# Kernel tuning notes

Measured on AMD Instinct MI355X. Metric: run time of the kernel, lower is better.

Reference implementation:

```python
import jax, jax.numpy as jnp
import numpy as np
from jax.ops import segment_sum

NUM_EMBEDDINGS = 512
EMBEDDING_DIM = 64
COMMITMENT_COST = 0.25
DECAY = 0.99
EPSILON = 1e-05


def setup_inputs() -> dict:
    key = jax.random.key(0)
    k1, k2, k3 = jax.random.split(key, 3)
    B, C, T = 32, EMBEDDING_DIM, 4096
    z = jax.random.normal(k1, (B, C, T), dtype=jnp.float32)
    embedding = jax.random.normal(k2, (NUM_EMBEDDINGS, EMBEDDING_DIM), dtype=jnp.float32)
    cluster_size = jnp.zeros((NUM_EMBEDDINGS,), dtype=jnp.float32)
    embed_avg = jax.random.normal(k3, (NUM_EMBEDDINGS, EMBEDDING_DIM), dtype=jnp.float32)
    return {"z": z, "embedding": embedding, "cluster_size": cluster_size, "embed_avg": embed_avg}


def reference(z, embedding, cluster_size, embed_avg):
    B, C, T = z.shape
    K = embedding.shape[0]
    # flatten: (B, C, T) -> (B*T, C), matching reshape(B,C,-1).permute(0,2,1).reshape(-1,C)
    z_flat = jnp.transpose(z, (0, 2, 1)).reshape(-1, C)  # [N, C]
    N = z_flat.shape[0]

    # squared-euclidean nearest-code search (argmin of cdist == argmin of sq dist)
    d2 = (jnp.sum(z_flat * z_flat, axis=1, keepdims=True)
          - 2.0 * (z_flat @ embedding.T)
          + jnp.sum(embedding * embedding, axis=1)[None, :])  # [N, K]
    indices = jnp.argmin(d2, axis=1)  # [N] int

    # quantize: gather instead of one-hot matmul (same math)
    quantized_flat = embedding[indices]  # [N, C]
    quantized = jnp.transpose(quantized_flat.reshape(B, T, C), (0, 2, 1))  # [B, C, T]

    # EMA codebook update (training branch)
    n = segment_sum(jnp.ones((N,), dtype=z.dtype), indices, num_segments=K)  # [K]
    new_cluster_size = cluster_size * DECAY + (1.0 - DECAY) * n
    embed_sum = segment_sum(z_flat, indices, num_segments=K)  # [K, C]
    new_embed_avg = embed_avg * DECAY + (1.0 - DECAY) * embed_sum
    n_tot = jnp.sum(new_cluster_size)
    cs_smoothed = (new_cluster_size + EPSILON) / (n_tot + K * EPSILON) * n_tot
    new_embedding = new_embed_avg / cs_smoothed[:, None]

    # commitment loss against detached quantized
    commitment_loss = jnp.mean((z - jax.lax.stop_gradient(quantized)) ** 2)
    vq_loss = COMMITMENT_COST * commitment_loss

    # straight-through estimator
    quantized_st = z + jax.lax.stop_gradient(quantized - z)

    # perplexity over code usage (zero-count codes contribute ~0, as in torch unique version)
    probs = n / N
    perplexity = jnp.exp(-jnp.sum(probs * jnp.log(probs + 1e-10)))

    return (quantized_st, indices, vq_loss, perplexity,
            new_embedding, new_cluster_size, new_embed_avg)
```

## Files before the change

### kernel.cpp

```cpp
#include <hip/hip_runtime.h>
#include <math.h>

#define KB_NUM 512
#define DIMC 64
#define BSZ 32
#define TLEN 4096
#define NTOK (BSZ * TLEN)
#define DECAY_F 0.99f
#define EPS_F 1e-5f

#define Q_OFF    ((size_t)0)
#define IDX_OFF  ((size_t)BSZ * DIMC * TLEN)
#define LOSS_OFF (IDX_OFF + (size_t)NTOK)
#define PLEX_OFF (LOSS_OFF + 1)
#define NEMB_OFF (PLEX_OFF + 1)
#define NCS_OFF  (NEMB_OFF + (size_t)KB_NUM * DIMC)
#define NEA_OFF  (NCS_OFF + (size_t)KB_NUM)

typedef _Float16 f16x8 __attribute__((ext_vector_type(8)));
typedef float    f32x4 __attribute__((ext_vector_type(4)));

__global__ __launch_bounds__(64) void vq_prep_e(
    const float* __restrict__ emb,
    _Float16* __restrict__ efrag,
    float* __restrict__ enorm)
{
    const int k = blockIdx.x;
    const int c = threadIdx.x;
    float v = emb[(size_t)k * DIMC + c];
    _Float16 h = (_Float16)v;
    _Float16 l = (_Float16)(v - (float)h);

    const int kgrp = k >> 4, row = k & 15;
    const int ks = c >> 5, seg = (c & 31) >> 3, j = c & 7;
    const int lane = seg * 16 + row;
    const size_t base = ((size_t)(kgrp * 2 + ks) * 2) * 512;
    efrag[base + (size_t)lane * 8 + j]       = h;
    efrag[base + 512 + (size_t)lane * 8 + j] = l;

    float s = v * v;
    #pragma unroll
    for (int off = 32; off > 0; off >>= 1)
        s += __shfl_down(s, off, 64);
    if (c == 0) enorm[k] = 0.5f * s;
}

#define LOADA(P, kg) do {                                                     \
    const _Float16* fb_ = efrag + ((size_t)((kg) & 31) * 4) * 512             \
                                + (size_t)ln * 8;                             \
    P##h0 = *(const f16x8*)(fb_);                                             \
    P##l0 = *(const f16x8*)(fb_ + 512);                                       \
    P##h1 = *(const f16x8*)(fb_ + 1024);                                      \
    P##l1 = *(const f16x8*)(fb_ + 1536);                                      \
} while (0)

#define CONSUME(P, ct) do {                                                   \
    _Pragma("unroll")                                                         \
    for (int tt = 0; tt < 4; ++tt)                                            \
        acc[ct][tt] = __builtin_amdgcn_mfma_f32_16x16x32_f16(                 \
            P##h0, zhf[tt][0], acc[ct][tt], 0, 0, 0);                         \
    _Pragma("unroll")                                                         \
    for (int tt = 0; tt < 4; ++tt)                                            \
        acc[ct][tt] = __builtin_amdgcn_mfma_f32_16x16x32_f16(                 \
            P##h0, zlf[tt][0], acc[ct][tt], 0, 0, 0);                         \
    _Pragma("unroll")                                                         \
    for (int tt = 0; tt < 4; ++tt)                                            \
        acc[ct][tt] = __builtin_amdgcn_mfma_f32_16x16x32_f16(                 \
            P##l0, zhf[tt][0], acc[ct][tt], 0, 0, 0);                         \
    _Pragma("unroll")                                                         \
    for (int tt = 0; tt < 4; ++tt)                                            \
        acc[ct][tt] = __builtin_amdgcn_mfma_f32_16x16x32_f16(                 \
            P##l0, zlf[tt][0], acc[ct][tt], 0, 0, 0);                         \
    _Pragma("unroll")                                                         \
    for (int tt = 0; tt < 4; ++tt)                                            \
        acc[ct][tt] = __builtin_amdgcn_mfma_f32_16x16x32_f16(                 \
            P##h1, zhf[tt][1], acc[ct][tt], 0, 0, 0);                         \
    _Pragma("unroll")                                                         \
    for (int tt = 0; tt < 4; ++tt)                                            \
        acc[ct][tt] = __builtin_amdgcn_mfma_f32_16x16x32_f16(                 \
            P##h1, zlf[tt][1], acc[ct][tt], 0, 0, 0);                         \
    _Pragma("unroll")                                                         \
    for (int tt = 0; tt < 4; ++tt)                                            \
        acc[ct][tt] = __builtin_amdgcn_mfma_f32_16x16x32_f16(                 \
            P##l1, zhf[tt][1], acc[ct][tt], 0, 0, 0);                         \
    _Pragma("unroll")                                                         \
    for (int tt = 0; tt < 4; ++tt)                                            \
        acc[ct][tt] = __builtin_amdgcn_mfma_f32_16x16x32_f16(                 \
            P##l1, zlf[tt][1], acc[ct][tt], 0, 0, 0);                         \
} while (0)

__global__ __launch_bounds__(256, 2) void vq_main_kernel(
    const float* __restrict__ z,
    const float* __restrict__ emb,
    const _Float16* __restrict__ efrag,
    const float* __restrict__ enorm,
    float* __restrict__ out,
    float* __restrict__ lossAcc)
{
    __shared__ float zs[256 * 65];
    __shared__ float sen[KB_NUM];

    const int tid = threadIdx.x;
    const int w   = tid >> 6;
    const int ln  = tid & 63;
    const int bk  = blockIdx.x;
    const int b   = bk >> 4;
    const int t0  = (bk & 15) << 8;

    sen[tid]       = enorm[tid];
    sen[tid + 256] = enorm[tid + 256];

    const float* zg = z + (size_t)b * (DIMC * TLEN) + t0;

    #pragma unroll 8
    for (int c = 0; c < DIMC; ++c)
        zs[tid * 65 + c] = zg[(size_t)c * TLEN + tid];
    __syncthreads();

    f16x8 zhf[4][2], zlf[4][2];
    #pragma unroll
    for (int tt = 0; tt < 4; ++tt) {
        #pragma unroll
        for (int ks = 0; ks < 2; ++ks) {
            const float* zrow = &zs[(w * 64 + tt * 16 + (ln & 15)) * 65
                                    + ks * 32 + ((ln >> 4) << 3)];
            #pragma unroll
            for (int j = 0; j < 8; ++j) {
                float v = zrow[j];
                _Float16 h = (_Float16)v;
                zhf[tt][ks][j] = h;
                zlf[tt][ks][j] = (_Float16)(v - (float)h);
            }
        }
    }

    float bv[4] = {3.4e38f, 3.4e38f, 3.4e38f, 3.4e38f};
    int   bi[4] = {0, 0, 0, 0};

    f16x8 A0h0, A0l0, A0h1, A0l1;
    f16x8 A1h0, A1l0, A1h1, A1l1;
    LOADA(A0, 0);
    LOADA(A1, 1);

    #pragma unroll 1
    for (int chunk = 0; chunk < 8; ++chunk) {
        const int kb = chunk * 4;
        f32x4 acc[4][4];
        #pragma unroll
        for (int ct = 0; ct < 4; ++ct)
            #pragma unroll
            for (int tt = 0; tt < 4; ++tt)
                acc[ct][tt] = (f32x4){0.f, 0.f, 0.f, 0.f};

        CONSUME(A0, 0); LOADA(A0, kb + 2);
        CONSUME(A1, 1); LOADA(A1, kb + 3);
        CONSUME(A0, 2); LOADA(A0, kb + 4);
        CONSUME(A1, 3); LOADA(A1, kb + 5);

        #pragma unroll
        for (int ct = 0; ct < 4; ++ct) {
            const int cb = chunk * 64 + ct * 16 + ((ln >> 4) << 2);
            float4 en = *(const float4*)&sen[cb];
            const float e0 = en.x, e1 = en.y, e2 = en.z, e3 = en.w;
            #pragma unroll
            for (int tt = 0; tt < 4; ++tt) {
                float s0 = e0 - acc[ct][tt][0];
                float s1 = e1 - acc[ct][tt][1];
                float s2 = e2 - acc[ct][tt][2];
                float s3 = e3 - acc[ct][tt][3];
                if (s0 < bv[tt]) { bv[tt] = s0; bi[tt] = cb; }
                if (s1 < bv[tt]) { bv[tt] = s1; bi[tt] = cb + 1; }
                if (s2 < bv[tt]) { bv[tt] = s2; bi[tt] = cb + 2; }
                if (s3 < bv[tt]) { bv[tt] = s3; bi[tt] = cb + 3; }
            }
        }
    }

    #pragma unroll
    for (int mask = 16; mask <= 32; mask <<= 1) {
        #pragma unroll
        for (int tt = 0; tt < 4; ++tt) {
            float ov = __shfl_xor(bv[tt], mask, 64);
            int   oi = __shfl_xor(bi[tt], mask, 64);
            if (ov < bv[tt] || (ov == bv[tt] && oi < bi[tt])) {
                bv[tt] = ov; bi[tt] = oi;
            }
        }
    }

    const int g = ln >> 4;
    const int idxv = (g == 0) ? bi[0] : (g == 1) ? bi[1] : (g == 2) ? bi[2] : bi[3];
    const int tok = w * 64 + ln;

    out[IDX_OFF + (size_t)b * TLEN + t0 + tok] = (float)idxv;

    const float* er   = emb + (size_t)idxv * DIMC;
    const float* zrow = &zs[tok * 65];
    float* qo = out + (size_t)b * (DIMC * TLEN) + t0 + tok;

    float lsum = 0.f;
    #pragma unroll
    for (int c4 = 0; c4 < DIMC / 4; ++c4) {
        float4 ev = *(const float4*)(er + c4 * 4);
        float z0 = zrow[c4 * 4 + 0], z1 = zrow[c4 * 4 + 1];
        float z2 = zrow[c4 * 4 + 2], z3 = zrow[c4 * 4 + 3];
        float d0 = ev.x - z0, d1 = ev.y - z1, d2 = ev.z - z2, d3 = ev.w - z3;
        qo[(size_t)(c4 * 4 + 0) * TLEN] = z0 + d0;
        qo[(size_t)(c4 * 4 + 1) * TLEN] = z1 + d1;
        qo[(size_t)(c4 * 4 + 2) * TLEN] = z2 + d2;
        qo[(size_t)(c4 * 4 + 3) * TLEN] = z3 + d3;
        lsum = fmaf(d0, d0, lsum); lsum = fmaf(d1, d1, lsum);
        lsum = fmaf(d2, d2, lsum); lsum = fmaf(d3, d3, lsum);
    }

    #pragma unroll
    for (int off = 32; off > 0; off >>= 1)
        lsum += __shfl_down(lsum, off, 64);
    if (ln == 0) atomicAdd(lossAcc, lsum);
}

__global__ __launch_bounds__(512, 1) void vq_bin_kernel(
    const float* __restrict__ z,
    const float* __restrict__ out,
    float* __restrict__ cnt,
    float* __restrict__ esum,
    int R)
{
    __shared__ float acc[KB_NUM][DIMC + 1];
    __shared__ float zs[64][DIMC + 1];
    __shared__ float scnt[KB_NUM];
    __shared__ int   idxbuf[64];

    const int tid = threadIdx.x;
    const int w   = tid >> 6;
    const int ln  = tid & 63;

    for (int j = tid; j < KB_NUM * (DIMC + 1); j += 512) ((float*)acc)[j] = 0.f;
    if (tid < KB_NUM) scnt[tid] = 0.f;
    __syncthreads();

    const int b   = blockIdx.x >> 3;
    const int tb  = (blockIdx.x & 7) * 512;
    const float* zp = z + (size_t)b * (DIMC * TLEN) + tb;
    const size_t gib = IDX_OFF + (size_t)b * TLEN + tb;

    #pragma unroll 1
    for (int ch = 0; ch < 8; ++ch) {
        const int t0 = ch * 64;
        {
            const int cb = w * 8;
            #pragma unroll
            for (int j = 0; j < 8; ++j) {
                const int c = cb + j;
                zs[ln][c] = zp[(size_t)c * TLEN + t0 + ln];
            }
            if (tid < 64)
                idxbuf[tid] = (int)out[gib + t0 + tid];
        }
        __syncthreads();

        #pragma unroll
        for (int i = 0; i < 8; ++i) {
            const int tok = w * 8 + i;
            const int idx = idxbuf[tok];
            float v = zs[tok][ln];
            atomicAdd(&acc[idx][ln], v);
            if (ln == 0) atomicAdd(&scnt[idx], 1.0f);
        }
        __syncthreads();
    }

    const int r = (int)((unsigned)blockIdx.x % (unsigned)R);
    for (int j = tid; j < KB_NUM * DIMC; j += 512) {
        const int k = j >> 6, c = j & 63;
        float v = acc[k][c];
        if (v != 0.f) atomicAdd(esum + (size_t)r * (KB_NUM * DIMC) + j, v);
    }
    if (tid < KB_NUM) {
        float v = scnt[tid];
        if (v != 0.f) atomicAdd(cnt + (size_t)r * KB_NUM + tid, v);
    }
}

__global__ __launch_bounds__(512) void vq_stats_kernel(
    const float* __restrict__ cluster_size,
    const float* __restrict__ cnt,
    const float* __restrict__ lossAcc,
    float* __restrict__ out,
    float* __restrict__ ntotp,
    int R)
{
    const int k = threadIdx.x;

    float n = 0.f;
    #pragma unroll 4
    for (int r = 0; r < R; ++r) n += cnt[(size_t)r * KB_NUM + k];

    float ncs = cluster_size[k] * DECAY_F + (1.0f - DECAY_F) * n;
    out[NCS_OFF + k] = ncs;

    __shared__ float red[KB_NUM];

    red[k] = ncs;
    __syncthreads();
    for (int s = KB_NUM / 2; s > 0; s >>= 1) {
        if (k < s) red[k] += red[k + s];
        __syncthreads();
    }
    if (k == 0) ntotp[0] = red[0];
    __syncthreads();

    float p = n * (1.0f / (float)NTOK);
    red[k] = p * logf(p + 1e-10f);
    __syncthreads();
    for (int s = KB_NUM / 2; s > 0; s >>= 1) {
        if (k < s) red[k] += red[k + s];
        __syncthreads();
    }
    if (k == 0) {
        out[PLEX_OFF] = expf(-red[0]);
        out[LOSS_OFF] = 0.25f * lossAcc[0] * (1.0f / (float)(BSZ * DIMC * TLEN));
    }
}

__global__ __launch_bounds__(64) void vq_embed_kernel(
    const float* __restrict__ embed_avg,
    const float* __restrict__ esum,
    const float* __restrict__ ntotp,
    float* __restrict__ out,
    int R)
{
    const int k = blockIdx.x;
    const int c = threadIdx.x;

    float es = 0.f;
    #pragma unroll 4
    for (int r = 0; r < R; ++r)
        es += esum[((size_t)r * KB_NUM + k) * DIMC + c];

    float nea = embed_avg[(size_t)k * DIMC + c] * DECAY_F + (1.0f - DECAY_F) * es;
    out[NEA_OFF + (size_t)k * DIMC + c] = nea;

    float ncs  = out[NCS_OFF + k];
    float ntot = ntotp[0];
    float denom = (ncs + EPS_F) / (ntot + (float)KB_NUM * EPS_F) * ntot;
    out[NEMB_OFF + (size_t)k * DIMC + c] = nea / denom;
}

extern "C" void kernel_launch(void* const* d_in, const int* in_sizes, int n_in,
                              void* d_out, int out_size, void* d_ws, size_t ws_size,
                              hipStream_t stream)
{
    const float* z            = (const float*)d_in[0];
    const float* emb          = (const float*)d_in[1];
    const float* cluster_size = (const float*)d_in[2];
    const float* embed_avg    = (const float*)d_in[3];
    float* out = (float*)d_out;

    char* ws = (char*)d_ws;
    float*     lossAcc = (float*)ws;
    float*     ntotp   = (float*)(ws + 64);
    float*     enorm   = (float*)(ws + 256);
    _Float16*  efrag   = (_Float16*)(ws + 4096);
    const size_t CNT_OFF = 4096 + 131072;
    const size_t perR = (size_t)(KB_NUM + KB_NUM * DIMC) * sizeof(float);

    int R = 1;
    if (ws_size > CNT_OFF + perR)
        R = (int)((ws_size - CNT_OFF) / perR);
    if (R < 1) R = 1;
    if (R > 16) R = 16;

    float* cnt  = (float*)(ws + CNT_OFF);
    float* esum = cnt + (size_t)R * KB_NUM;

    hipMemsetAsync(ws, 0, CNT_OFF + (size_t)R * perR, stream);

    vq_prep_e<<<dim3(KB_NUM), dim3(DIMC), 0, stream>>>(emb, efrag, enorm);

    vq_main_kernel<<<dim3(NTOK / 256), dim3(256), 0, stream>>>(
        z, emb, efrag, enorm, out, lossAcc);

    vq_bin_kernel<<<dim3(NTOK / 512), dim3(512), 0, stream>>>(z, out, cnt, esum, R);

    vq_stats_kernel<<<dim3(1), dim3(512), 0, stream>>>(
        cluster_size, cnt, lossAcc, out, ntotp, R);

    vq_embed_kernel<<<dim3(KB_NUM), dim3(DIMC), 0, stream>>>(
        embed_avg, esum, ntotp, out, R);
}
```

Measured before the change: 141.3 us.

## Write token-major z copy in main kernel and bin from it

The main kernel already stages z in shared memory, and now also writes a transposed token-major copy of it (32 MB) to workspace. A new binning kernel reads that copy with coalesced per-token rows and broadcasts indices by shuffle, replacing the strided channel-major reads and the chunked shared-memory staging with its barriers. In exchange it adds 32 MB of extra global writes plus a re-read, and it needs a large workspace. When the workspace is too small the old path is used.

```diff
diff --git a/kernel.cpp b/kernel.cpp
--- a/kernel.cpp
+++ b/kernel.cpp
@@ -95,7 +95,8 @@
     const _Float16* __restrict__ efrag,
     const float* __restrict__ enorm,
     float* __restrict__ out,
-    float* __restrict__ lossAcc)
+    float* __restrict__ lossAcc,
+    float* __restrict__ zt)
 {
     __shared__ float zs[256 * 65];
     __shared__ float sen[KB_NUM];
@@ -116,6 +117,18 @@
     for (int c = 0; c < DIMC; ++c)
         zs[tid * 65 + c] = zg[(size_t)c * TLEN + tid];
     __syncthreads();
+
+    if (zt != nullptr) {
+        float* ztb = zt + ((size_t)b * TLEN + t0) * DIMC;
+        #pragma unroll
+        for (int s = 0; s < 16; ++s) {
+            const int f    = s * 256 + tid;
+            const int trow = f >> 4;
+            const int c4   = f & 15;
+            float4 v = *(const float4*)&zs[trow * 65 + c4 * 4];
+            *(float4*)(ztb + (size_t)trow * DIMC + c4 * 4) = v;
+        }
+    }
 
     f16x8 zhf[4][2], zlf[4][2];
     #pragma unroll
@@ -219,6 +232,47 @@
     if (ln == 0) atomicAdd(lossAcc, lsum);
 }
 
+__global__ __launch_bounds__(512, 1) void vq_bin2_kernel(
+    const float* __restrict__ zt,
+    const float* __restrict__ out,
+    float* __restrict__ cnt,
+    float* __restrict__ esum,
+    int R)
+{
+    __shared__ float acc[KB_NUM][DIMC];
+    __shared__ float scnt[KB_NUM];
+
+    const int tid = threadIdx.x;
+    const int w   = tid >> 6;
+    const int ln  = tid & 63;
+
+    for (int j = tid; j < KB_NUM * DIMC; j += 512) ((float*)acc)[j] = 0.f;
+    if (tid < KB_NUM) scnt[tid] = 0.f;
+    __syncthreads();
+
+    const int tokbase = blockIdx.x * 512 + w * 64;
+    const int myidx = (int)out[IDX_OFF + tokbase + ln];
+
+    #pragma unroll 8
+    for (int i = 0; i < 64; ++i) {
+        const int idx = __shfl(myidx, i, 64);
+        float v = zt[(size_t)(tokbase + i) * DIMC + ln];
+        atomicAdd(&acc[idx][ln], v);
+        if (ln == 0) atomicAdd(&scnt[idx], 1.0f);
+    }
+    __syncthreads();
+
+    const int r = (int)((unsigned)blockIdx.x % (unsigned)R);
+    for (int j = tid; j < KB_NUM * DIMC; j += 512) {
+        float v = ((const float*)acc)[j];
+        if (v != 0.f) atomicAdd(esum + (size_t)r * (KB_NUM * DIMC) + j, v);
+    }
+    if (tid < KB_NUM) {
+        float v = scnt[tid];
+        if (v != 0.f) atomicAdd(cnt + (size_t)r * KB_NUM + tid, v);
+    }
+}
+
 __global__ __launch_bounds__(512, 1) void vq_bin_kernel(
     const float* __restrict__ z,
     const float* __restrict__ out,
@@ -227,7 +281,7 @@
     int R)
 {
     __shared__ float acc[KB_NUM][DIMC + 1];
-    __shared__ float zs[64][DIMC + 1];
+    __shared__ float zsb[64][DIMC + 1];
     __shared__ float scnt[KB_NUM];
     __shared__ int   idxbuf[64];
 
@@ -252,18 +306,17 @@
             #pragma unroll
             for (int j = 0; j < 8; ++j) {
                 const int c = cb + j;
-                zs[ln][c] = zp[(size_t)c * TLEN + t0 + ln];
+                zsb[ln][c] = zp[(size_t)c * TLEN + t0 + ln];
             }
             if (tid < 64)
                 idxbuf[tid] = (int)out[gib + t0 + tid];
         }
         __syncthreads();
-
         #pragma unroll
         for (int i = 0; i < 8; ++i) {
             const int tok = w * 8 + i;
             const int idx = idxbuf[tok];
-            float v = zs[tok][ln];
+            float v = zsb[tok][ln];
             atomicAdd(&acc[idx][ln], v);
             if (ln == 0) atomicAdd(&scnt[idx], 1.0f);
         }
@@ -364,12 +417,24 @@
     _Float16*  efrag   = (_Float16*)(ws + 4096);
     const size_t CNT_OFF = 4096 + 131072;
     const size_t perR = (size_t)(KB_NUM + KB_NUM * DIMC) * sizeof(float);
+    const size_t zt_bytes = (size_t)NTOK * DIMC * sizeof(float);
 
     int R = 1;
-    if (ws_size > CNT_OFF + perR)
-        R = (int)((ws_size - CNT_OFF) / perR);
-    if (R < 1) R = 1;
-    if (R > 16) R = 16;
+    float* zt = nullptr;
+    {
+        long long avail = (long long)ws_size - (long long)CNT_OFF
+                        - (long long)zt_bytes;
+        if (avail >= 4 * (long long)perR) {
+            R = (int)(avail / (long long)perR);
+            if (R > 16) R = 16;
+            zt = (float*)(ws + CNT_OFF + (size_t)R * perR);
+        } else {
+            if (ws_size > CNT_OFF + perR)
+                R = (int)((ws_size - CNT_OFF) / perR);
+            if (R < 1) R = 1;
+            if (R > 16) R = 16;
+        }
+    }
 
     float* cnt  = (float*)(ws + CNT_OFF);
     float* esum = cnt + (size_t)R * KB_NUM;
@@ -379,9 +444,14 @@
     vq_prep_e<<<dim3(KB_NUM), dim3(DIMC), 0, stream>>>(emb, efrag, enorm);
 
     vq_main_kernel<<<dim3(NTOK / 256), dim3(256), 0, stream>>>(
-        z, emb, efrag, enorm, out, lossAcc);
-
-    vq_bin_kernel<<<dim3(NTOK / 512), dim3(512), 0, stream>>>(z, out, cnt, esum, R);
+        z, emb, efrag, enorm, out, lossAcc, zt);
+
+    if (zt != nullptr)
+        vq_bin2_kernel<<<dim3(NTOK / 512), dim3(512), 0, stream>>>(
+            zt, out, cnt, esum, R);
+    else
+        vq_bin_kernel<<<dim3(NTOK / 512), dim3(512), 0, stream>>>(
+            z, out, cnt, esum, R);
 
     vq_stats_kernel<<<dim3(1), dim3(512), 0, stream>>>(
         cluster_size, cnt, lossAcc, out, ntotp, R);
```

Result: no change. 139.8 us (-1.0%).
